# Kernel optimization log

Hardware: AMD Instinct MI355X
Metric: run time of the kernel (lower is better)

The kernel has to match this reference:

```python
import jax, jax.numpy as jnp
import numpy as np

NUM_FIELDS = 39
PER_FIELD_VOCAB = 10000
TOTAL_VOCAB = NUM_FIELDS * PER_FIELD_VOCAB
EMBED_DIM = 128
DIM_INT = (2, 3)
RANKS = (128, 128)
BATCH = 2048


def setup_inputs() -> dict:
    key = jax.random.key(0)
    k_x, k_emb, k_lin, k_b, k_w0, k_w1 = jax.random.split(key, 6)
    x = jax.random.randint(k_x, (BATCH, NUM_FIELDS), 0, PER_FIELD_VOCAB, dtype=jnp.int64 if jax.config.jax_enable_x64 else jnp.int32)
    embed_table = jax.random.normal(k_emb, (TOTAL_VOCAB, EMBED_DIM), dtype=jnp.float32) * 0.01
    linear_table = jax.random.normal(k_lin, (TOTAL_VOCAB, 1), dtype=jnp.float32) * 0.01
    bias = jnp.zeros((1,), dtype=jnp.float32)
    # trunc_normal_(std=0.01) approximated by scaled normal (same distribution family)
    W0 = jax.random.normal(k_w0, (DIM_INT[0], RANKS[0], NUM_FIELDS), dtype=jnp.float32) * 0.01
    W1 = jax.random.normal(k_w1, (DIM_INT[1], RANKS[1], NUM_FIELDS), dtype=jnp.float32) * 0.01
    return {"x": x, "embed_table": embed_table, "linear_table": linear_table,
            "bias": bias, "W0": W0, "W1": W1}


def _calc_cross(emb, W):
    # emb: [B, F, D]; W: [L, R, F]
    # dot_products[b,d,r,l] = sum_f W[l,r,f] * emb[b,f,d]   (torch: 'bljk,bki->bijl')
    dp = jnp.einsum('lrf,bfd->bdrl', W, emb)          # [B, D, R, L]
    prod_over_l = jnp.prod(dp, axis=3)                # [B, D, R]
    return jnp.sum(prod_over_l, axis=(1, 2))[:, None]  # [B, 1]


def reference(x, embed_table, linear_table, bias, W0, W1):
    # per-field offsets into the flat embedding table (FeaturesEmbedding behavior)
    offsets = (jnp.arange(NUM_FIELDS) * PER_FIELD_VOCAB).astype(x.dtype)
    idx = x + offsets[None, :]                        # [B, F]
    emb = embed_table[idx]                            # [B, F, D]
    # FeaturesLinear: sum of per-feature weights + bias -> [B, 1]
    ret = jnp.sum(linear_table[idx], axis=1) + bias
    for W in (W0, W1):
        ret = ret + _calc_cross(emb, W)
    return (ret, 0)
```

## Files before the change

### kernel.cpp

```cpp
#include <hip/hip_runtime.h>
#include <hip/hip_bf16.h>

#define NUM_FIELDS 39
#define PER_FIELD_VOCAB 10000
#define EMBED_DIM 128
#define RANK 128
#define BATCH 2048
#define ET_STRIDE 72

typedef __bf16 bf16x8 __attribute__((ext_vector_type(8)));
typedef __bf16 bf16x4 __attribute__((ext_vector_type(4)));
typedef float  f32x4  __attribute__((ext_vector_type(4)));
typedef float  f32x4u __attribute__((ext_vector_type(4), aligned(4)));
typedef float  f32x2u __attribute__((ext_vector_type(2), aligned(4)));

__device__ inline bf16x8 load_afrag(const float* __restrict__ Wrow, int quad, int kc) {
    if (kc == 0) {
        f32x4u a = *reinterpret_cast<const f32x4u*>(Wrow + quad * 8);
        f32x4u b = *reinterpret_cast<const f32x4u*>(Wrow + quad * 8 + 4);
        return (bf16x8){(__bf16)a[0], (__bf16)a[1], (__bf16)a[2], (__bf16)a[3],
                        (__bf16)b[0], (__bf16)b[1], (__bf16)b[2], (__bf16)b[3]};
    }
    if (quad == 0) {
        f32x4u a = *reinterpret_cast<const f32x4u*>(Wrow + 32);
        f32x2u b = *reinterpret_cast<const f32x2u*>(Wrow + 36);
        float  c = Wrow[38];
        return (bf16x8){(__bf16)a[0], (__bf16)a[1], (__bf16)a[2], (__bf16)a[3],
                        (__bf16)b[0], (__bf16)b[1], (__bf16)c, (__bf16)0.f};
    }
    return (bf16x8){(__bf16)0.f, (__bf16)0.f, (__bf16)0.f, (__bf16)0.f,
                    (__bf16)0.f, (__bf16)0.f, (__bf16)0.f, (__bf16)0.f};
}

__global__ __launch_bounds__(256) void tfm_fused(const int* __restrict__ x,
                                                 const float* __restrict__ embed_table,
                                                 const float* __restrict__ linear_table,
                                                 const float* __restrict__ bias,
                                                 const float* __restrict__ W0,
                                                 const float* __restrict__ W1,
                                                 float* __restrict__ out,
                                                 int out_size) {
    __shared__ int sidx[NUM_FIELDS];
    __shared__ __align__(16) __bf16 eT[EMBED_DIM * ET_STRIDE];
    __shared__ float wpart[4];

    const int tid = threadIdx.x;
    const int b   = blockIdx.x;

    if (tid < NUM_FIELDS)
        sidx[tid] = x[b * NUM_FIELDS + tid] + tid * PER_FIELD_VOCAB;
    __syncthreads();

#pragma unroll
    for (int i = 0; i < 8; ++i) {
        int k  = tid + i * 256;
        int d  = k & (EMBED_DIM - 1);
        int fq = k >> 7;
        float v[4];
#pragma unroll
        for (int c = 0; c < 4; ++c) {
            int f = fq * 4 + c;
            v[c] = (f < NUM_FIELDS) ? embed_table[(size_t)sidx[f] * EMBED_DIM + d] : 0.f;
        }
        bf16x4 pk = {(__bf16)v[0], (__bf16)v[1], (__bf16)v[2], (__bf16)v[3]};
        int fg  = fq >> 1;
        int grp = (fg + 2 * d) & 7;
        *reinterpret_cast<bf16x4*>(reinterpret_cast<char*>(eT)
            + d * (ET_STRIDE * 2) + grp * 16 + (fq & 1) * 8) = pk;
    }

    float partial = (tid < NUM_FIELDS) ? linear_table[sidx[tid]] : 0.f;
    __syncthreads();

    const int wave = tid >> 6, lane = tid & 63;
    const int m = lane & 15, quad = lane >> 4;

    float pairp = 0.f, trip = 0.f;

    for (int rti = 0; rti < 2; ++rti) {
        const int r = (wave * 2 + rti) * 16 + m;

        bf16x8 af[5][2];
#pragma unroll
        for (int l = 0; l < 2; ++l) {
            const float* Wrow = W0 + ((size_t)(l * RANK) + r) * NUM_FIELDS;
#pragma unroll
            for (int kc = 0; kc < 2; ++kc) af[l][kc] = load_afrag(Wrow, quad, kc);
        }
#pragma unroll
        for (int l = 0; l < 3; ++l) {
            const float* Wrow = W1 + ((size_t)(l * RANK) + r) * NUM_FIELDS;
#pragma unroll
            for (int kc = 0; kc < 2; ++kc) af[2 + l][kc] = load_afrag(Wrow, quad, kc);
        }

        for (int dt = 0; dt < 8; ++dt) {
            const int d = dt * 16 + m;
            bf16x8 bfrag[2];
#pragma unroll
            for (int kc = 0; kc < 2; ++kc) {
                int grp = ((kc * 4 + quad) + 2 * d) & 7;
                bfrag[kc] = *reinterpret_cast<const bf16x8*>(
                    reinterpret_cast<const char*>(eT) + d * (ET_STRIDE * 2) + grp * 16);
            }
            f32x4 acc[5];
#pragma unroll
            for (int l = 0; l < 5; ++l) acc[l] = (f32x4){0.f, 0.f, 0.f, 0.f};
#pragma unroll
            for (int kc = 0; kc < 2; ++kc)
#pragma unroll
                for (int l = 0; l < 5; ++l)
                    acc[l] = __builtin_amdgcn_mfma_f32_16x16x32_bf16(
                        af[l][kc], bfrag[kc], acc[l], 0, 0, 0);
#pragma unroll
            for (int i = 0; i < 4; ++i) {
                pairp += acc[0][i] * acc[1][i];
                trip  += acc[2][i] * acc[3][i] * acc[4][i];
            }
        }
    }

    partial += pairp + trip;

#pragma unroll
    for (int off = 32; off > 0; off >>= 1)
        partial += __shfl_down(partial, off, 64);
    if (lane == 0) wpart[wave] = partial;
    __syncthreads();
    if (tid == 0)
        out[b] = wpart[0] + wpart[1] + wpart[2] + wpart[3] + bias[0];

    if (b == 0)
        for (int j = BATCH + tid; j < out_size; j += 256)
            out[j] = 0.f;
}

extern "C" void kernel_launch(void* const* d_in, const int* in_sizes, int n_in,
                              void* d_out, int out_size, void* d_ws, size_t ws_size,
                              hipStream_t stream) {
    const int*   x            = (const int*)d_in[0];
    const float* embed_table  = (const float*)d_in[1];
    const float* linear_table = (const float*)d_in[2];
    const float* bias         = (const float*)d_in[3];
    const float* W0           = (const float*)d_in[4];
    const float* W1           = (const float*)d_in[5];

    tfm_fused<<<BATCH, 256, 0, stream>>>(x, embed_table, linear_table, bias, W0, W1,
                                         (float*)d_out, out_size);
}
```

Baseline: 330.7 us.

## Split gather into separate kernel staging bf16 transposed embeddings in workspace

Splits the fused kernel in two. The first kernel gathers embedding rows, converts them to bf16, transposes them through LDS and writes a per-sample image to the global workspace. The second kernel reads its MFMA B fragments straight from that global image, with no LDS staging or barrier. The aim is to separate the latency-bound gather from the MFMA phase so each kernel can run at better occupancy, at the cost of an extra global write and read (about 32KB per sample) and a second launch.

```diff
diff --git a/kernel.cpp b/kernel.cpp
--- a/kernel.cpp
+++ b/kernel.cpp
@@ -6,13 +6,52 @@
 #define EMBED_DIM 128
 #define RANK 128
 #define BATCH 2048
-#define ET_STRIDE 72
+#define LDS_ROW 144
+#define IMG_ROW 128
+#define IMG_BYTES (EMBED_DIM * IMG_ROW)
 
 typedef __bf16 bf16x8 __attribute__((ext_vector_type(8)));
-typedef __bf16 bf16x4 __attribute__((ext_vector_type(4)));
 typedef float  f32x4  __attribute__((ext_vector_type(4)));
 typedef float  f32x4u __attribute__((ext_vector_type(4), aligned(4)));
 typedef float  f32x2u __attribute__((ext_vector_type(2), aligned(4)));
+
+__global__ __launch_bounds__(256) void gather_t(const int* __restrict__ x,
+                                                const float* __restrict__ embed_table,
+                                                __bf16* __restrict__ ws) {
+    __shared__ int sidx[NUM_FIELDS];
+    __shared__ __align__(16) char eT[EMBED_DIM * LDS_ROW];
+
+    const int tid = threadIdx.x, b = blockIdx.x;
+    if (tid < NUM_FIELDS)
+        sidx[tid] = x[b * NUM_FIELDS + tid] + tid * PER_FIELD_VOCAB;
+    __syncthreads();
+
+    const int d = tid & (EMBED_DIM - 1);
+    const int half = tid >> 7;
+
+    float v[32];
+#pragma unroll
+    for (int j = 0; j < 32; ++j) {
+        int f = half * 32 + j;
+        v[j] = (f < NUM_FIELDS) ? embed_table[(size_t)sidx[f] * EMBED_DIM + d] : 0.f;
+    }
+#pragma unroll
+    for (int g = 0; g < 4; ++g) {
+        bf16x8 pk = {(__bf16)v[g*8+0], (__bf16)v[g*8+1], (__bf16)v[g*8+2], (__bf16)v[g*8+3],
+                     (__bf16)v[g*8+4], (__bf16)v[g*8+5], (__bf16)v[g*8+6], (__bf16)v[g*8+7]};
+        *reinterpret_cast<bf16x8*>(eT + d * LDS_ROW + half * 64 + g * 16) = pk;
+    }
+    __syncthreads();
+
+    const int o  = tid * 64;
+    const int dd = o >> 7, rest = o & (IMG_ROW - 1);
+    char* dst = (char*)ws + (size_t)b * IMG_BYTES + o;
+#pragma unroll
+    for (int j = 0; j < 4; ++j) {
+        uint4 val = *reinterpret_cast<const uint4*>(eT + dd * LDS_ROW + rest + j * 16);
+        *reinterpret_cast<uint4*>(dst + j * 16) = val;
+    }
+}
 
 __device__ inline bf16x8 load_afrag(const float* __restrict__ Wrow, int quad, int kc) {
     if (kc == 0) {
@@ -32,51 +71,27 @@
                     (__bf16)0.f, (__bf16)0.f, (__bf16)0.f, (__bf16)0.f};
 }
 
-__global__ __launch_bounds__(256) void tfm_fused(const int* __restrict__ x,
-                                                 const float* __restrict__ embed_table,
-                                                 const float* __restrict__ linear_table,
-                                                 const float* __restrict__ bias,
-                                                 const float* __restrict__ W0,
-                                                 const float* __restrict__ W1,
-                                                 float* __restrict__ out,
-                                                 int out_size) {
-    __shared__ int sidx[NUM_FIELDS];
-    __shared__ __align__(16) __bf16 eT[EMBED_DIM * ET_STRIDE];
+__global__ __launch_bounds__(256) void tfm_compute(const int* __restrict__ x,
+                                                   const __bf16* __restrict__ ws,
+                                                   const float* __restrict__ linear_table,
+                                                   const float* __restrict__ bias,
+                                                   const float* __restrict__ W0,
+                                                   const float* __restrict__ W1,
+                                                   float* __restrict__ out,
+                                                   int out_size) {
     __shared__ float wpart[4];
 
-    const int tid = threadIdx.x;
-    const int b   = blockIdx.x;
-
-    if (tid < NUM_FIELDS)
-        sidx[tid] = x[b * NUM_FIELDS + tid] + tid * PER_FIELD_VOCAB;
-    __syncthreads();
-
-#pragma unroll
-    for (int i = 0; i < 8; ++i) {
-        int k  = tid + i * 256;
-        int d  = k & (EMBED_DIM - 1);
-        int fq = k >> 7;
-        float v[4];
-#pragma unroll
-        for (int c = 0; c < 4; ++c) {
-            int f = fq * 4 + c;
-            v[c] = (f < NUM_FIELDS) ? embed_table[(size_t)sidx[f] * EMBED_DIM + d] : 0.f;
-        }
-        bf16x4 pk = {(__bf16)v[0], (__bf16)v[1], (__bf16)v[2], (__bf16)v[3]};
-        int fg  = fq >> 1;
-        int grp = (fg + 2 * d) & 7;
-        *reinterpret_cast<bf16x4*>(reinterpret_cast<char*>(eT)
-            + d * (ET_STRIDE * 2) + grp * 16 + (fq & 1) * 8) = pk;
-    }
-
-    float partial = (tid < NUM_FIELDS) ? linear_table[sidx[tid]] : 0.f;
-    __syncthreads();
-
+    const int tid = threadIdx.x, b = blockIdx.x;
     const int wave = tid >> 6, lane = tid & 63;
     const int m = lane & 15, quad = lane >> 4;
 
+    float partial = 0.f;
+    if (tid < NUM_FIELDS)
+        partial = linear_table[x[b * NUM_FIELDS + tid] + tid * PER_FIELD_VOCAB];
+
+    const char* img = (const char*)ws + (size_t)b * IMG_BYTES;
+
     float pairp = 0.f, trip = 0.f;
-
     for (int rti = 0; rti < 2; ++rti) {
         const int r = (wave * 2 + rti) * 16 + m;
 
@@ -98,11 +113,10 @@
             const int d = dt * 16 + m;
             bf16x8 bfrag[2];
 #pragma unroll
-            for (int kc = 0; kc < 2; ++kc) {
-                int grp = ((kc * 4 + quad) + 2 * d) & 7;
+            for (int kc = 0; kc < 2; ++kc)
                 bfrag[kc] = *reinterpret_cast<const bf16x8*>(
-                    reinterpret_cast<const char*>(eT) + d * (ET_STRIDE * 2) + grp * 16);
-            }
+                    img + d * IMG_ROW + kc * 64 + quad * 16);
+
             f32x4 acc[5];
 #pragma unroll
             for (int l = 0; l < 5; ++l) acc[l] = (f32x4){0.f, 0.f, 0.f, 0.f};
@@ -119,7 +133,6 @@
             }
         }
     }
-
     partial += pairp + trip;
 
 #pragma unroll
@@ -144,7 +157,9 @@
     const float* bias         = (const float*)d_in[3];
     const float* W0           = (const float*)d_in[4];
     const float* W1           = (const float*)d_in[5];
+    __bf16* ws = (__bf16*)d_ws;
 
-    tfm_fused<<<BATCH, 256, 0, stream>>>(x, embed_table, linear_table, bias, W0, W1,
-                                         (float*)d_out, out_size);
+    gather_t<<<BATCH, 256, 0, stream>>>(x, embed_table, ws);
+    tfm_compute<<<BATCH, 256, 0, stream>>>(x, ws, linear_table, bias, W0, W1,
+                                           (float*)d_out, out_size);
 }
```

Result: faster. 323.5 us (-2.2%).
